# Kernel optimization log

Hardware: AMD Instinct MI355X
Metric: run time of the kernel (lower is better)

## Reference

```python
import jax, jax.numpy as jnp
import numpy as np

K = 4          # Chebyshev order
N = 8192       # nodes
I = 128        # input_size
H = 256        # hidden_size
E = 262144     # nnz in Laplacian


def _uniform(key, shape, bound):
    return jax.random.uniform(key, shape, jnp.float32, -bound, bound)


def setup_inputs() -> dict:
    key = jax.random.key(0)
    ks = jax.random.split(key, 20)
    bound = np.sqrt(1.0 / I)
    inp = {
        "x": jax.random.normal(ks[0], (N, I), jnp.float32),
        "h": jax.random.normal(ks[1], (N, H), jnp.float32),
        "c": jax.random.normal(ks[2], (N, H), jnp.float32),
        "lap_vals": 0.1 * jax.random.normal(ks[3], (E,), jnp.float32),
        "pos": jax.random.randint(ks[4], (E, 2), 0, N, jnp.int64),
        "W_fh": _uniform(ks[5], (K, H, H), bound),
        "W_fx": _uniform(ks[6], (K, H, I), bound),
        "bf": _uniform(ks[7], (N, H), bound),
        "W_ih": _uniform(ks[8], (K, H, H), bound),
        "W_ix": _uniform(ks[9], (K, H, I), bound),
        "bi": _uniform(ks[10], (N, H), bound),
        "W_oh": _uniform(ks[11], (K, H, H), bound),
        "W_ox": _uniform(ks[12], (K, H, I), bound),
        "bo": _uniform(ks[13], (N, H), bound),
        "W_ch": _uniform(ks[14], (K, H, H), bound),
        "W_cx": _uniform(ks[15], (K, H, I), bound),
        "bc": _uniform(ks[16], (N, H), bound),
    }
    return inp


def cheb_features(L, X):
    # T_k(L) @ X via the 3-term recurrence applied to vectors (no N x N powers).
    Ts = [X, L @ X]
    for _ in range(2, K):
        Ts.append(2.0 * (L @ Ts[-1]) - Ts[-2])
    return jnp.stack(Ts[:K])  # [K, N, F]


def graph_conv(TX, W):
    # sum_k T_k(L) X W_k^T ; TX: [K,N,F], W: [K,H,F] -> [N,H]
    return jnp.einsum("knf,khf->nh", TX, W)


def reference(x, h, c, lap_vals, pos, W_fh, W_fx, bf, W_ih, W_ix, bi,
              W_oh, W_ox, bo, W_ch, W_cx, bc):
    L = jnp.zeros((N, N), jnp.float32).at[pos[:, 0], pos[:, 1]].set(lap_vals)
    Th = cheb_features(L, h)  # [K,N,H]
    Tx = cheb_features(L, x)  # [K,N,I]
    f = jax.nn.sigmoid(graph_conv(Th, W_fh) + graph_conv(Tx, W_fx) + bf)
    i = jax.nn.sigmoid(graph_conv(Th, W_ih) + graph_conv(Tx, W_ix) + bi)
    o = jax.nn.sigmoid(graph_conv(Th, W_oh) + graph_conv(Tx, W_ox) + bo)
    c_new = i * jnp.tanh(graph_conv(Th, W_ch) + graph_conv(Tx, W_cx) + bc) + f * c
    h_new = o * jnp.tanh(c_new)
    return (h_new, c_new)
```

## Files before the change

### kernel.cpp

```cpp
#include <hip/hip_runtime.h>
#include <hip/hip_bf16.h>
#include <cstdint>

#define NN 8192
#define HH 256
#define II 128
#define KORD 4
#define EE 262144
#define KW 1536
#define MW 1024
#define RCAP 128
#define BK 64

typedef __attribute__((ext_vector_type(8))) short bf16x8;
typedef __attribute__((ext_vector_type(8))) unsigned short u16x8;
typedef __attribute__((ext_vector_type(4))) float f32x4;

__device__ __forceinline__ float bf2f(unsigned short u) {
    union { uint32_t i; float f; } x; x.i = ((uint32_t)u) << 16; return x.f;
}
__device__ __forceinline__ unsigned short f2bf(float f) {
    __hip_bfloat16 b = __float2bfloat16(f);
    return *(unsigned short*)&b;
}

__device__ __forceinline__ void read_pos(const int* __restrict__ pos, int flag,
                                         int e, int& r, int& c) {
    if (flag) { r = pos[4 * e]; c = pos[4 * e + 2]; }
    else      { r = pos[2 * e]; c = pos[2 * e + 1]; }
}

__global__ void init_small(uint32_t* __restrict__ rcnt,
                           const int* __restrict__ pos, int* __restrict__ flag) {
    int i = blockIdx.x * blockDim.x + threadIdx.x;
    if (i < NN) rcnt[i] = 0u;
    if (i == 0) {
        int f = 1;
        for (int k = 0; k < 128; ++k) {
            if (pos[2 * k + 1] != 0) { f = 0; break; }
        }
        *flag = f;
    }
}

__global__ void scatter_fixed(const int* __restrict__ pos, const int* __restrict__ flagp,
                              const float* __restrict__ lap,
                              uint32_t* __restrict__ rcnt, uint2* __restrict__ cpack) {
    int e = blockIdx.x * blockDim.x + threadIdx.x;
    if (e >= EE) return;
    int flag = *flagp;
    int r, c; read_pos(pos, flag, e, r, c);
    uint32_t slot = atomicAdd(&rcnt[r], 1u);
    if (slot < RCAP) {
        uint2 p;
        p.x = ((uint32_t)(e + 1) << 13) | (uint32_t)c;
        p.y = __float_as_uint(lap[e]);
        cpack[(size_t)r * RCAP + slot] = p;
    }
}

__global__ __launch_bounds__(256) void dedup_rows(uint32_t* __restrict__ rcnt,
                                                  const uint2* __restrict__ cpack,
                                                  uint32_t* __restrict__ cpk) {
    int r = blockIdx.x * 4 + (threadIdx.x >> 6);
    int lane = threadIdx.x & 63;
    uint32_t lenu = rcnt[r];
    int len = (lenu > RCAP) ? RCAP : (int)lenu;
    const uint2* base = &cpack[(size_t)r * RCAP];
    uint32_t m0 = 0u, m1 = 0u;
    float v0 = 0.0f, v1 = 0.0f;
    if (lane < len) { uint2 p = base[lane]; m0 = p.x; v0 = __uint_as_float(p.y); }
    if (64 + lane < len) { uint2 p = base[64 + lane]; m1 = p.x; v1 = __uint_as_float(p.y); }
    bool lose0 = false, lose1 = false;
    int nchunk = (len + 63) >> 6;
    for (int ch = 0; ch < nchunk; ++ch) {
        int cl = len - ch * 64; if (cl > 64) cl = 64;
        for (int i = 0; i < cl; ++i) {
            uint32_t mi = __shfl(ch == 0 ? m0 : m1, i);
            lose0 |= (((mi ^ m0) & 8191u) == 0u) && (mi > m0);
            lose1 |= (((mi ^ m1) & 8191u) == 0u) && (mi > m1);
        }
    }
    uint32_t* ob = &cpk[(size_t)r * RCAP];
    if (lane < len)
        ob[lane] = ((uint32_t)f2bf(lose0 ? 0.0f : v0) << 16) | (m0 & 8191u);
    if (64 + lane < len)
        ob[64 + lane] = ((uint32_t)f2bf(lose1 ? 0.0f : v1) << 16) | (m1 & 8191u);
    if (lane == 0 && lenu > RCAP) rcnt[r] = RCAP;
}

template <int F>
__device__ __forceinline__ void spmv_seg(
    const uint32_t* __restrict__ rcnt, const uint32_t* __restrict__ cpk,
    unsigned short* Am, int cbsrc, int cbprev, int cbdst,
    float a, float b, int r, int lane) {
    uint32_t len = rcnt[r]; if (len > RCAP) len = RCAP;
    uint32_t s = (uint32_t)r * RCAP, e = s + len;
    int off = lane * 8;
    float acc[8];
#pragma unroll
    for (int j = 0; j < 8; ++j) acc[j] = 0.0f;
    uint32_t i = s;
    for (; i + 4 <= e; i += 4) {
        uint32_t p0 = cpk[i], p1 = cpk[i + 1], p2 = cpk[i + 2], p3 = cpk[i + 3];
        u16x8 g0 = *(const u16x8*)&Am[(size_t)(p0 & 8191u) * KW + cbsrc + off];
        u16x8 g1 = *(const u16x8*)&Am[(size_t)(p1 & 8191u) * KW + cbsrc + off];
        u16x8 g2 = *(const u16x8*)&Am[(size_t)(p2 & 8191u) * KW + cbsrc + off];
        u16x8 g3 = *(const u16x8*)&Am[(size_t)(p3 & 8191u) * KW + cbsrc + off];
        float v0 = bf2f((unsigned short)(p0 >> 16));
        float v1 = bf2f((unsigned short)(p1 >> 16));
        float v2 = bf2f((unsigned short)(p2 >> 16));
        float v3 = bf2f((unsigned short)(p3 >> 16));
#pragma unroll
        for (int j = 0; j < 8; ++j)
            acc[j] += v0 * bf2f(g0[j]) + v1 * bf2f(g1[j]) +
                      v2 * bf2f(g2[j]) + v3 * bf2f(g3[j]);
    }
    for (; i < e; ++i) {
        uint32_t p0 = cpk[i];
        u16x8 g0 = *(const u16x8*)&Am[(size_t)(p0 & 8191u) * KW + cbsrc + off];
        float v0 = bf2f((unsigned short)(p0 >> 16));
#pragma unroll
        for (int j = 0; j < 8; ++j) acc[j] += v0 * bf2f(g0[j]);
    }
    u16x8 ob;
    if (b != 0.0f) {
        u16x8 pv = *(const u16x8*)&Am[(size_t)r * KW + cbprev + off];
#pragma unroll
        for (int j = 0; j < 8; ++j) ob[j] = f2bf(a * acc[j] + b * bf2f(pv[j]));
    } else {
#pragma unroll
        for (int j = 0; j < 8; ++j) ob[j] = f2bf(a * acc[j]);
    }
    *(u16x8*)&Am[(size_t)r * KW + cbdst + off] = ob;
}

#define NBH (NN / 8)
#define NBX (NN / 16)
__global__ __launch_bounds__(256) void spmv_cheb_dual(
    const uint32_t* __restrict__ rcnt, const uint32_t* __restrict__ cpk,
    unsigned short* Am,
    int sh, int ph, int dh,
    int sx, int px, int dx,
    float a, float b) {
    int bid = blockIdx.x, t = threadIdx.x;
    if (bid < NBH) {
        int r = bid * 8 + (t >> 5), lane = t & 31;
        spmv_seg<HH>(rcnt, cpk, Am, sh, ph, dh, a, b, r, lane);
    } else {
        int r = (bid - NBH) * 16 + (t >> 4), lane = t & 15;
        spmv_seg<II>(rcnt, cpk, Am, sx, px, dx, a, b, r, lane);
    }
}

__global__ void pack_T0(const float* __restrict__ h, const float* __restrict__ x,
                        unsigned short* __restrict__ Am) {
    int idx = blockIdx.x * blockDim.x + threadIdx.x;
    if (idx >= NN * 96) return;
    int n, q, col;
    const float* src;
    if (idx < NN * 64) { n = idx >> 6; q = (idx & 63) * 4; src = &h[(size_t)n * HH + q]; col = q; }
    else { int ix = idx - NN * 64; n = ix >> 5; q = (ix & 31) * 4; src = &x[(size_t)n * II + q]; col = 1024 + q; }
    float4 v = *(const float4*)src;
    ushort4 pk;
    pk.x = f2bf(v.x); pk.y = f2bf(v.y); pk.z = f2bf(v.z); pk.w = f2bf(v.w);
    *(ushort4*)&Am[(size_t)n * KW + col] = pk;
}

__global__ void pack_B(const float* __restrict__ Wfh, const float* __restrict__ Wih,
                       const float* __restrict__ Woh, const float* __restrict__ Wch,
                       const float* __restrict__ Wfx, const float* __restrict__ Wix,
                       const float* __restrict__ Wox, const float* __restrict__ Wcx,
                       __hip_bfloat16* __restrict__ Bm) {
    int idx = blockIdx.x * blockDim.x + threadIdx.x;
    if (idx >= MW * KW) return;
    int m = idx / KW, j = idx - m * KW;
    int g = m >> 8, hh = m & 255;
    const float* Wh = (g == 0) ? Wfh : (g == 1) ? Wih : (g == 2) ? Woh : Wch;
    const float* Wx = (g == 0) ? Wfx : (g == 1) ? Wix : (g == 2) ? Wox : Wcx;
    float v;
    if (j < 1024) { int k = j >> 8, f = j & 255; v = Wh[((size_t)k * HH + hh) * HH + f]; }
    else { int jj = j - 1024; int k = jj >> 7, f = jj & 127; v = Wx[((size_t)k * HH + hh) * II + f]; }
    Bm[idx] = __float2bfloat16(v);
}

__device__ __forceinline__ void gload_lds16(const void* g, void* l) {
    __builtin_amdgcn_global_load_lds(
        (const __attribute__((address_space(1))) void*)g,
        (__attribute__((address_space(3))) void*)l, 16, 0, 0);
}

__device__ __forceinline__ void stage_side(const __hip_bfloat16* __restrict__ G,
                                           int r0, int kk, int t, short* lds) {
#pragma unroll
    for (int s = 0; s < 4; ++s) {
        int e = (s * 256 + t) * 8;
        int row = e >> 6;
        int kks = ((((e >> 3) & 7) ^ (row & 7)) << 3);
        gload_lds16(&G[(size_t)(r0 + row) * KW + kk + kks], &lds[e]);
    }
}

__global__ __launch_bounds__(256) void gemm_mfma(
    const __hip_bfloat16* __restrict__ A,
    const __hip_bfloat16* __restrict__ B,
    float* __restrict__ C) {
    __shared__ short Alds[2][128 * BK];
    __shared__ short Blds[2][128 * BK];
    int bid = blockIdx.x;
    int sw = (bid & 7) * 64 + (bid >> 3);
    int m0 = (sw & 7) * 128;
    int n0 = (sw >> 3) * 128;
    int t = threadIdx.x;
    int w = t >> 6, l = t & 63;
    int wr = w >> 1, wc = w & 1;
    int lrow = l & 15, q = l >> 4;

    f32x4 acc[4][4];
#pragma unroll
    for (int i = 0; i < 4; ++i)
#pragma unroll
        for (int j = 0; j < 4; ++j) acc[i][j] = (f32x4)0.0f;

    stage_side(A, n0, 0, t, Alds[0]);
    stage_side(B, m0, 0, t, Blds[0]);
    __syncthreads();

    int cur = 0;
    for (int k0 = 0; k0 < KW; k0 += BK) {
        if (k0 + BK < KW) {
            stage_side(A, n0, k0 + BK, t, Alds[cur ^ 1]);
            stage_side(B, m0, k0 + BK, t, Blds[cur ^ 1]);
        }
#pragma unroll
        for (int h = 0; h < 2; ++h) {
            int sl = (((h << 2) | q) ^ (lrow & 7)) << 3;
            bf16x8 af[4], bfr[4];
#pragma unroll
            for (int i = 0; i < 4; ++i)
                af[i] = *(const bf16x8*)&Alds[cur][(wr * 64 + i * 16 + lrow) * BK + sl];
#pragma unroll
            for (int j = 0; j < 4; ++j)
                bfr[j] = *(const bf16x8*)&Blds[cur][(wc * 64 + j * 16 + lrow) * BK + sl];
#pragma unroll
            for (int i = 0; i < 4; ++i)
#pragma unroll
                for (int j = 0; j < 4; ++j)
                    acc[i][j] = __builtin_amdgcn_mfma_f32_16x16x32_bf16(af[i], bfr[j], acc[i][j], 0, 0, 0);
        }
        __syncthreads();
        cur ^= 1;
    }

    int r4 = (l >> 4) * 4;
#pragma unroll
    for (int i = 0; i < 4; ++i)
#pragma unroll
        for (int j = 0; j < 4; ++j)
#pragma unroll
            for (int r = 0; r < 4; ++r) {
                int row = n0 + wr * 64 + i * 16 + r4 + r;
                int col = m0 + wc * 64 + j * 16 + lrow;
                C[(size_t)row * MW + col] = acc[i][j][r];
            }
}

__device__ __forceinline__ float sigmoidf_(float x) { return 1.0f / (1.0f + expf(-x)); }

__global__ __launch_bounds__(256) void lstm_ew(
    const float* __restrict__ C,
    const float* __restrict__ bf, const float* __restrict__ bi,
    const float* __restrict__ bo, const float* __restrict__ bc,
    const float* __restrict__ cin, float* __restrict__ out) {
    int i = blockIdx.x * blockDim.x + threadIdx.x;
    if (i >= NN * HH / 4) return;
    int n = i >> 6;
    int h4 = (i & 63) * 4;
    size_t cb = (size_t)n * MW;
    size_t hb = (size_t)n * HH + h4;
    float4 pf = *(const float4*)&C[cb + 0 * HH + h4];
    float4 pi = *(const float4*)&C[cb + 1 * HH + h4];
    float4 po = *(const float4*)&C[cb + 2 * HH + h4];
    float4 pc = *(const float4*)&C[cb + 3 * HH + h4];
    float4 vbf = *(const float4*)&bf[hb];
    float4 vbi = *(const float4*)&bi[hb];
    float4 vbo = *(const float4*)&bo[hb];
    float4 vbc = *(const float4*)&bc[hb];
    float4 vc  = *(const float4*)&cin[hb];
    float4 hn, cn;
    {
        float fg = sigmoidf_(pf.x + vbf.x), ig = sigmoidf_(pi.x + vbi.x);
        float og = sigmoidf_(po.x + vbo.x), cg = tanhf(pc.x + vbc.x);
        cn.x = ig * cg + fg * vc.x; hn.x = og * tanhf(cn.x);
    }
    {
        float fg = sigmoidf_(pf.y + vbf.y), ig = sigmoidf_(pi.y + vbi.y);
        float og = sigmoidf_(po.y + vbo.y), cg = tanhf(pc.y + vbc.y);
        cn.y = ig * cg + fg * vc.y; hn.y = og * tanhf(cn.y);
    }
    {
        float fg = sigmoidf_(pf.z + vbf.z), ig = sigmoidf_(pi.z + vbi.z);
        float og = sigmoidf_(po.z + vbo.z), cg = tanhf(pc.z + vbc.z);
        cn.z = ig * cg + fg * vc.z; hn.z = og * tanhf(cn.z);
    }
    {
        float fg = sigmoidf_(pf.w + vbf.w), ig = sigmoidf_(pi.w + vbi.w);
        float og = sigmoidf_(po.w + vbo.w), cg = tanhf(pc.w + vbc.w);
        cn.w = ig * cg + fg * vc.w; hn.w = og * tanhf(cn.w);
    }
    *(float4*)&out[hb] = hn;
    *(float4*)&out[(size_t)NN * HH + hb] = cn;
}

extern "C" void kernel_launch(void* const* d_in, const int* in_sizes, int n_in,
                              void* d_out, int out_size, void* d_ws, size_t ws_size,
                              hipStream_t stream) {
    const float* x   = (const float*)d_in[0];
    const float* h   = (const float*)d_in[1];
    const float* c   = (const float*)d_in[2];
    const float* lap = (const float*)d_in[3];
    const int*   pos = (const int*)d_in[4];
    const float* Wfh = (const float*)d_in[5];
    const float* Wfx = (const float*)d_in[6];
    const float* bf  = (const float*)d_in[7];
    const float* Wih = (const float*)d_in[8];
    const float* Wix = (const float*)d_in[9];
    const float* bi  = (const float*)d_in[10];
    const float* Woh = (const float*)d_in[11];
    const float* Wox = (const float*)d_in[12];
    const float* bo  = (const float*)d_in[13];
    const float* Wch = (const float*)d_in[14];
    const float* Wcx = (const float*)d_in[15];
    const float* bc  = (const float*)d_in[16];
    float* out = (float*)d_out;

    uint8_t* ws = (uint8_t*)d_ws;
    size_t off = 0;
    auto take = [&](size_t bytes) -> void* {
        void* p = ws + off;
        off += (bytes + 255) & ~(size_t)255;
        return p;
    };
    int*      flag = (int*)take(4);
    uint32_t* rcnt = (uint32_t*)take((size_t)NN * 4);
    uint2*    cpack= (uint2*)take((size_t)NN * RCAP * 8);
    uint32_t* cpk  = (uint32_t*)take((size_t)NN * RCAP * 4);
    unsigned short* Amat = (unsigned short*)take((size_t)NN * KW * 2);
    __hip_bfloat16* Bmat = (__hip_bfloat16*)take((size_t)MW * KW * 2);
    float*    Cpre = (float*)take((size_t)NN * MW * 4);

    init_small<<<NN / 256, 256, 0, stream>>>(rcnt, pos, flag);
    scatter_fixed<<<EE / 256, 256, 0, stream>>>(pos, flag, lap, rcnt, cpack);
    dedup_rows<<<NN / 4, 256, 0, stream>>>(rcnt, cpack, cpk);

    pack_T0<<<(NN * 96 + 255) / 256, 256, 0, stream>>>(h, x, Amat);
    pack_B<<<(MW * KW + 255) / 256, 256, 0, stream>>>(Wfh, Wih, Woh, Wch,
                                                      Wfx, Wix, Wox, Wcx, Bmat);

    int sg = NBH + NBX;
    spmv_cheb_dual<<<sg, 256, 0, stream>>>(rcnt, cpk, Amat,
        0, 0, 256, 1024, 1024, 1152, 1.0f, 0.0f);
    spmv_cheb_dual<<<sg, 256, 0, stream>>>(rcnt, cpk, Amat,
        256, 0, 512, 1152, 1024, 1280, 2.0f, -1.0f);
    spmv_cheb_dual<<<sg, 256, 0, stream>>>(rcnt, cpk, Amat,
        512, 256, 768, 1280, 1152, 1408, 2.0f, -1.0f);

    gemm_mfma<<<512, 256, 0, stream>>>((const __hip_bfloat16*)Amat, Bmat, Cpre);

    lstm_ew<<<(NN * HH / 4 + 255) / 256, 256, 0, stream>>>(Cpre, bf, bi, bo, bc, c, out);
}
```

Baseline: 164.1 us.

## Split SpMV and T0 packing into column slices for L2 locality

The SpMV kernel now gives each block one 32-column (h) or 16-column (x) slice for 64 or 128 rows, with 4 or 2 threads per row, instead of covering all columns of a few rows. Blocks with the same slice index touch only that slice of the gathered source rows, which is meant to shrink the working set seen by cache and raise hit rates on the random gathers. pack_T0 is reordered the same way, by column slice. In exchange, each row's nonzero list (cpk) is now read 8 times, once per slice, and each thread still handles 8 contiguous bf16 values per gather.

```diff
diff --git a/kernel.cpp b/kernel.cpp
--- a/kernel.cpp
+++ b/kernel.cpp
@@ -89,7 +89,6 @@
     if (lane == 0 && lenu > RCAP) rcnt[r] = RCAP;
 }
 
-template <int F>
 __device__ __forceinline__ void spmv_seg(
     const uint32_t* __restrict__ rcnt, const uint32_t* __restrict__ cpk,
     unsigned short* Am, int cbsrc, int cbprev, int cbdst,
@@ -135,8 +134,6 @@
     *(u16x8*)&Am[(size_t)r * KW + cbdst + off] = ob;
 }
 
-#define NBH (NN / 8)
-#define NBX (NN / 16)
 __global__ __launch_bounds__(256) void spmv_cheb_dual(
     const uint32_t* __restrict__ rcnt, const uint32_t* __restrict__ cpk,
     unsigned short* Am,
@@ -144,23 +141,38 @@
     int sx, int px, int dx,
     float a, float b) {
     int bid = blockIdx.x, t = threadIdx.x;
-    if (bid < NBH) {
-        int r = bid * 8 + (t >> 5), lane = t & 31;
-        spmv_seg<HH>(rcnt, cpk, Am, sh, ph, dh, a, b, r, lane);
+    if (bid < 1024) {
+        int s = (bid & 7) * 32;
+        int r = (bid >> 3) * 64 + (t >> 2);
+        int lane = t & 3;
+        spmv_seg(rcnt, cpk, Am, sh + s, ph + s, dh + s, a, b, r, lane);
     } else {
-        int r = (bid - NBH) * 16 + (t >> 4), lane = t & 15;
-        spmv_seg<II>(rcnt, cpk, Am, sx, px, dx, a, b, r, lane);
+        int b2 = bid - 1024;
+        int s = (b2 & 7) * 16;
+        int r = (b2 >> 3) * 128 + (t >> 1);
+        int lane = t & 1;
+        spmv_seg(rcnt, cpk, Am, sx + s, px + s, dx + s, a, b, r, lane);
     }
 }
 
 __global__ void pack_T0(const float* __restrict__ h, const float* __restrict__ x,
                         unsigned short* __restrict__ Am) {
-    int idx = blockIdx.x * blockDim.x + threadIdx.x;
-    if (idx >= NN * 96) return;
-    int n, q, col;
+    int bid = blockIdx.x;
+    int s = bid & 7;
+    int u = (bid >> 3) * 256 + threadIdx.x;
+    int n, col;
     const float* src;
-    if (idx < NN * 64) { n = idx >> 6; q = (idx & 63) * 4; src = &h[(size_t)n * HH + q]; col = q; }
-    else { int ix = idx - NN * 64; n = ix >> 5; q = (ix & 31) * 4; src = &x[(size_t)n * II + q]; col = 1024 + q; }
+    if (u < 65536) {
+        n = u >> 3;
+        col = s * 32 + (u & 7) * 4;
+        src = &h[(size_t)n * HH + col];
+    } else {
+        int u2 = u - 65536;
+        n = u2 >> 2;
+        int cx = s * 16 + (u2 & 3) * 4;
+        src = &x[(size_t)n * II + cx];
+        col = 1024 + cx;
+    }
     float4 v = *(const float4*)src;
     ushort4 pk;
     pk.x = f2bf(v.x); pk.y = f2bf(v.y); pk.z = f2bf(v.z); pk.w = f2bf(v.w);
@@ -353,11 +365,11 @@
     scatter_fixed<<<EE / 256, 256, 0, stream>>>(pos, flag, lap, rcnt, cpack);
     dedup_rows<<<NN / 4, 256, 0, stream>>>(rcnt, cpack, cpk);
 
-    pack_T0<<<(NN * 96 + 255) / 256, 256, 0, stream>>>(h, x, Amat);
+    pack_T0<<<3072, 256, 0, stream>>>(h, x, Amat);
     pack_B<<<(MW * KW + 255) / 256, 256, 0, stream>>>(Wfh, Wih, Woh, Wch,
                                                       Wfx, Wix, Wox, Wcx, Bmat);
 
-    int sg = NBH + NBX;
+    int sg = 1024 + 512;
     spmv_cheb_dual<<<sg, 256, 0, stream>>>(rcnt, cpk, Amat,
         0, 0, 256, 1024, 1024, 1152, 1.0f, 0.0f);
     spmv_cheb_dual<<<sg, 256, 0, stream>>>(rcnt, cpk, Amat,
```

New measurement: 193.1 us. +17.7%, slower.
